# Optimization experiments

Measured on AMD Instinct MI355X. Metric: run time of the kernel, lower is better.

## Reference

```python
import math
import jax, jax.numpy as jnp
import numpy as np

B, S, D, H, FF, E, V, RH = 8, 256, 512, 8, 2048, 8, 32000, 256
MAX_PATH, MAX_VISITS = 4, 2
NEG = -1e9
DH = D // H


def _make_pe():
    # PositionalEncoding buffer (sin/cos), sliced to seq len S
    pos = np.arange(S, dtype=np.float32)[:, None]
    div = np.exp(np.arange(0, D, 2, dtype=np.float32) * (-math.log(10000.0) / D))
    pe = np.zeros((S, D), dtype=np.float32)
    pe[:, 0::2] = np.sin(pos * div)
    pe[:, 1::2] = np.cos(pos * div)
    return jnp.asarray(pe[None])  # [1,S,D]


def setup_inputs() -> dict:
    key = jax.random.key(0)
    ks = jax.random.split(key, 12)
    s = 0.02
    return dict(
        input_ids=jax.random.randint(ks[0], (B, S), 0, V),
        emb=jax.random.normal(ks[1], (V, D), jnp.float32) * s,
        pe=_make_pe(),
        Wqkv=jax.random.normal(ks[2], (E, 3 * D, D), jnp.float32) * s,
        bqkv=jnp.zeros((E, 3 * D), jnp.float32),
        Wo=jax.random.normal(ks[3], (E, D, D), jnp.float32) * s,
        bo=jnp.zeros((E, D), jnp.float32),
        W1=jax.random.normal(ks[4], (E, FF, D), jnp.float32) * s,
        b1=jnp.zeros((E, FF), jnp.float32),
        W2=jax.random.normal(ks[5], (E, D, FF), jnp.float32) * s,
        b2=jnp.zeros((E, D), jnp.float32),
        ln1_g=jnp.ones((E, D), jnp.float32), ln1_b=jnp.zeros((E, D), jnp.float32),
        ln2_g=jnp.ones((E, D), jnp.float32), ln2_b=jnp.zeros((E, D), jnp.float32),
        tag=jax.random.normal(ks[6], (E, D), jnp.float32) * 0.01,
        r_w1=jax.random.normal(ks[7], (RH, D), jnp.float32) * s,
        r_b1=jnp.zeros((RH,), jnp.float32),
        r_w2=jax.random.normal(ks[8], (E + 1, RH), jnp.float32) * s,
        r_b2=jnp.zeros((E + 1,), jnp.float32),
        lm_w=jax.random.normal(ks[9], (V, D), jnp.float32) * s,
        lm_b=jnp.zeros((V,), jnp.float32),
    )


def _ln(x, g, b):
    # per-sample gathered LayerNorm params g,b: [B,D]; x: [B,S,D]
    mu = x.mean(-1, keepdims=True)
    var = ((x - mu) ** 2).mean(-1, keepdims=True)
    return (x - mu) * jax.lax.rsqrt(var + 1e-5) * g[:, None, :] + b[:, None, :]


def _expert(x, idx, Wqkv, bqkv, Wo, bo, W1, b1, W2, b2, g1, be1, g2, be2, tag):
    # post-norm TransformerEncoderLayer (eval mode, dropout off) with per-sample expert params
    qkv = jnp.einsum('bsd,bfd->bsf', x, Wqkv[idx]) + bqkv[idx][:, None, :]
    q, k, v = jnp.split(qkv, 3, axis=-1)
    q = q.reshape(B, S, H, DH)
    k = k.reshape(B, S, H, DH)
    v = v.reshape(B, S, H, DH)
    att = jax.nn.softmax(jnp.einsum('bqhd,bkhd->bhqk', q, k) / math.sqrt(DH), axis=-1)
    ctx = jnp.einsum('bhqk,bkhd->bqhd', att, v).reshape(B, S, D)
    attn_out = jnp.einsum('bsd,bod->bso', ctx, Wo[idx]) + bo[idx][:, None, :]
    x = _ln(x + attn_out, g1[idx], be1[idx])
    hid = jax.nn.relu(jnp.einsum('bsd,bfd->bsf', x, W1[idx]) + b1[idx][:, None, :])
    ff = jnp.einsum('bsf,bdf->bsd', hid, W2[idx]) + b2[idx][:, None, :]
    x = _ln(x + ff, g2[idx], be2[idx])
    return x + tag[idx][:, None, :]  # + specialization_tag


def reference(input_ids, emb, pe, Wqkv, bqkv, Wo, bo, W1, b1, W2, b2,
              ln1_g, ln1_b, ln2_g, ln2_b, tag, r_w1, r_b1, r_w2, r_b2, lm_w, lm_b):
    pad_mask = (jnp.arange(V) != 0).astype(emb.dtype)[:, None]  # padding_idx=0 row is zero
    rep = (emb * pad_mask)[input_ids] * math.sqrt(D) + pe[:, :S]
    visits = jnp.zeros((B, E), jnp.int32)
    active = jnp.ones((B,), bool)
    ent_total = jnp.asarray(0.0, rep.dtype)
    for _ in range(MAX_PATH):
        summary = rep.mean(1)  # [B,D]
        h = jax.nn.relu(summary @ r_w1.T + r_b1)
        logits = h @ r_w2.T + r_b2  # [B,E+1], last slot = terminate
        logits = jnp.concatenate(
            [jnp.where(visits >= MAX_VISITS, NEG, logits[:, :E]), logits[:, E:]], axis=1)
        probs = jax.nn.softmax(logits, axis=-1)
        ent = -jnp.sum(probs * jnp.log(probs + 1e-9), axis=-1)
        cnt = jnp.sum(active)
        ent_total = ent_total + jnp.where(
            cnt > 0, jnp.sum(ent * active) / jnp.maximum(cnt, 1).astype(ent.dtype), 0.0)
        choice = jnp.argmax(logits, axis=-1)       # eval mode: hard argmax
        go = active & (choice < E)                 # samples routed to an expert this step
        idx = jnp.where(go, choice, 0)
        visits = visits + jax.nn.one_hot(idx, E, dtype=jnp.int32) * go[:, None].astype(jnp.int32)
        new_rep = _expert(rep, idx, Wqkv, bqkv, Wo, bo, W1, b1, W2, b2,
                          ln1_g, ln1_b, ln2_g, ln2_b, tag)
        rep = jnp.where(go[:, None, None], new_rep, rep)  # terminated/inactive reps frozen
        active = go
    logits_lm = rep @ lm_w.T + lm_b  # [B,S,V]
    return logits_lm, ent_total
```

## Files before the change

### kernel.cpp

```cpp
#include <hip/hip_runtime.h>
#include <hip/hip_bf16.h>

#define NB 8
#define NS 256
#define ND 512
#define NH 8
#define NDH 64
#define NFF 2048
#define NE 8
#define NV 32000
#define NRH 256
#define MAXV 2
#define NEGV (-1e9f)

typedef __attribute__((ext_vector_type(8))) short short8;
typedef __attribute__((ext_vector_type(4))) float f32x4;

__device__ __forceinline__ unsigned short f2bf(float x) {
  unsigned int u = __float_as_uint(x);
  u = (u + 0x7fffu + ((u >> 16) & 1u)) >> 16;
  return (unsigned short)u;
}

__device__ __forceinline__ void gload16(const unsigned short* g, unsigned short* l) {
  __builtin_amdgcn_global_load_lds(
      (const __attribute__((address_space(1))) unsigned int*)g,
      (__attribute__((address_space(3))) unsigned int*)l, 16, 0, 0);
}

__device__ __forceinline__ int swzc(int lane) {
  return (lane & 3) ^ ((lane >> 3) & 3);
}

__device__ __forceinline__ void cast8(const float* s, unsigned short* d, int j) {
  const float4* s4 = (const float4*)s;
  float4 a = s4[j * 2], b = s4[j * 2 + 1];
  short8 v;
  v[0] = (short)f2bf(a.x); v[1] = (short)f2bf(a.y);
  v[2] = (short)f2bf(a.z); v[3] = (short)f2bf(a.w);
  v[4] = (short)f2bf(b.x); v[5] = (short)f2bf(b.y);
  v[6] = (short)f2bf(b.z); v[7] = (short)f2bf(b.w);
  *(short8*)&d[(size_t)j * 8] = v;
}

__global__ __launch_bounds__(256) void k_cast5e(
    const float* s0, unsigned short* d0, int n0,
    const float* s1, unsigned short* d1, int n1,
    const float* s2, unsigned short* d2, int n2,
    const float* s3, unsigned short* d3, int n3,
    const float* s4, unsigned short* d4, int n4,
    int nbcast,
    const int* __restrict__ ids, const float* __restrict__ emb,
    const float* __restrict__ pe, float* __restrict__ rep,
    unsigned short* __restrict__ repb, float* __restrict__ partial,
    int* visits, int* active, float* entp) {
  if (blockIdx.x == 0) {
    if (threadIdx.x < NB * NE) visits[threadIdx.x] = 0;
    if (threadIdx.x < NB) active[threadIdx.x] = 1;
    if (threadIdx.x == 0) *entp = 0.f;
  }
  if ((int)blockIdx.x >= nbcast) {
    int j2 = blockIdx.x - nbcast;
    int rg = j2 & 15, b = j2 >> 4;
    int t = threadIdx.x;
    int c0 = t, c1 = t + 256;
    float pa0 = 0.f, pa1 = 0.f, pb0 = 0.f, pb1 = 0.f;
    for (int row = 0; row < 16; ++row) {
      int s = rg * 16 + row;
      int id = ids[b * NS + s];
      float sc = (id != 0) ? 22.627416997969522f : 0.f;
      float v0 = emb[(size_t)id * ND + c0] * sc + pe[(size_t)s * ND + c0];
      float v1 = emb[(size_t)id * ND + c1] * sc + pe[(size_t)s * ND + c1];
      size_t base = ((size_t)b * NS + s) * ND;
      rep[base + c0] = v0; rep[base + c1] = v1;
      repb[base + c0] = f2bf(v0); repb[base + c1] = f2bf(v1);
      if (row < 8) { pa0 += v0; pa1 += v1; } else { pb0 += v0; pb1 += v1; }
    }
    float* ppa = partial + ((size_t)b * 32 + rg * 2) * ND;
    float* ppb = ppa + ND;
    ppa[c0] = pa0; ppa[c1] = pa1;
    ppb[c0] = pb0; ppb[c1] = pb1;
    return;
  }
  int j = blockIdx.x * 256 + threadIdx.x;
  if (j < n0) { cast8(s0, d0, j); return; }
  j -= n0;
  if (j < n1) { cast8(s1, d1, j); return; }
  j -= n1;
  if (j < n2) { cast8(s2, d2, j); return; }
  j -= n2;
  if (j < n3) { cast8(s3, d3, j); return; }
  j -= n3;
  if (j < n4) cast8(s4, d4, j);
}

__global__ __launch_bounds__(256) void k_router8(
    const float* __restrict__ partial,
    const float* __restrict__ rw1, const float* __restrict__ rb1,
    const float* __restrict__ rw2, const float* __restrict__ rb2,
    int* visits, const int* __restrict__ active_in, int* active_out,
    int* idx, int* go, float* ent_total) {
  int b = blockIdx.x;
  __shared__ float sm[ND];
  __shared__ float h[NRH];
  __shared__ float lg[NE + 1];
  __shared__ int scnt;
  int t = threadIdx.x;
  for (int i = t; i < ND; i += 256) {
    const float* pp = partial + ((size_t)b * 32) * ND + i;
    float s = 0.f;
#pragma unroll
    for (int rg = 0; rg < 32; ++rg) s += pp[(size_t)rg * ND];
    sm[i] = s * (1.f / NS);
  }
  if (t == 0) {
    int c = 0;
    for (int bb = 0; bb < NB; ++bb) c += active_in[bb];
    scnt = c;
  }
  __syncthreads();
  {
    const float* w = rw1 + (size_t)t * ND;
    float acc = rb1[t];
    for (int d = 0; d < ND; ++d) acc += sm[d] * w[d];
    h[t] = fmaxf(acc, 0.f);
  }
  __syncthreads();
  if (t < NE + 1) {
    const float* w = rw2 + t * NRH;
    float a = rb2[t];
    for (int r = 0; r < NRH; ++r) a += h[r] * w[r];
    lg[t] = a;
  }
  __syncthreads();
  if (t == 0) {
    int aprev = active_in[b];
    float l[NE + 1];
    for (int e = 0; e < NE; ++e)
      l[e] = (visits[b * NE + e] >= MAXV) ? NEGV : lg[e];
    l[NE] = lg[NE];
    float m = l[0];
    for (int e = 1; e <= NE; ++e) m = fmaxf(m, l[e]);
    float z = 0.f, p[NE + 1];
    for (int e = 0; e <= NE; ++e) { p[e] = __expf(l[e] - m); z += p[e]; }
    float zi = 1.f / z, ent = 0.f;
    for (int e = 0; e <= NE; ++e) {
      float pp = p[e] * zi;
      ent -= pp * __logf(pp + 1e-9f);
    }
    if (aprev && scnt > 0) atomicAdd(ent_total, ent / (float)scnt);
    int ch = 0; float bm = l[0];
    for (int e = 1; e <= NE; ++e) if (l[e] > bm) { bm = l[e]; ch = e; }
    int g = (aprev && ch < NE) ? 1 : 0;
    int ix = g ? ch : 0;
    visits[b * NE + ix] += g;
    idx[b] = ix; go[b] = g; active_out[b] = g;
  }
}

template <int OUT, int RELU, int SK>
__global__ __launch_bounds__(256) void k_gemm64p(
    const unsigned short* __restrict__ Aall, int sa,
    const unsigned short* __restrict__ Wall, const float* __restrict__ ball,
    float* __restrict__ Pall, unsigned short* __restrict__ Uall, int so,
    int N, int K,
    unsigned short* __restrict__ Qb, unsigned short* __restrict__ Kb,
    unsigned short* __restrict__ Vt,
    const int* __restrict__ go, const int* __restrict__ idx) {
  int b = blockIdx.z;
  if (!go[b]) return;
  int t = threadIdx.x;
  int lane = t & 63, w = t >> 6;
  int wm = (w >> 1) * 32, wn = (w & 1) * 32;
  int kc = blockIdx.x >> 2;
  int bm = (blockIdx.x & 3) * 64, bn = blockIdx.y * 64;
  int KC = K / SK;
  int lrow = (lane >> 4) * 4, lcol = lane & 15;
  const unsigned short* A = Aall + (size_t)b * sa + kc * KC;
  const unsigned short* W = Wall + (size_t)idx[b] * N * K + kc * KC;

  __shared__ __align__(16) unsigned short As[2][64][64];
  __shared__ __align__(16) unsigned short Bs[2][64][64];
  f32x4 acc[2][2];
#pragma unroll
  for (int i = 0; i < 2; ++i)
#pragma unroll
    for (int j = 0; j < 2; ++j) acc[i][j] = (f32x4){0.f, 0.f, 0.f, 0.f};

  int ch8 = (lane & 7) ^ ((lane >> 3) & 7);
  const unsigned short* ga = A + (size_t)(bm + w * 16 + (lane >> 3)) * K + ch8 * 8;
  const unsigned short* gb = W + (size_t)(bn + w * 16 + (lane >> 3)) * K + ch8 * 8;

#define ISSUE64(slot, kt)                                            \
  gload16(ga + (size_t)(kt) * 64, &As[slot][w * 16][0]);             \
  gload16(ga + (size_t)(kt) * 64 + 8 * (size_t)K, &As[slot][w * 16 + 8][0]); \
  gload16(gb + (size_t)(kt) * 64, &Bs[slot][w * 16][0]);             \
  gload16(gb + (size_t)(kt) * 64 + 8 * (size_t)K, &Bs[slot][w * 16 + 8][0]);

  int nk = KC >> 6;
  ISSUE64(0, 0)
  ISSUE64(1, 1)

  int row0 = lane & 15, g = lane >> 4;
  for (int it = 0; it < nk; ++it) {
    if (it < nk - 1) asm volatile("s_waitcnt vmcnt(4)" ::: "memory");
    else             asm volatile("s_waitcnt vmcnt(0)" ::: "memory");
    asm volatile("s_barrier" ::: "memory");
    int sl = it & 1;
    __builtin_amdgcn_s_setprio(1);
#pragma unroll
    for (int kk = 0; kk < 2; ++kk) {
      int co = ((kk * 4 + g) ^ (row0 & 7)) * 8;
      short8 a0 = *(const short8*)&As[sl][wm + row0][co];
      short8 a1 = *(const short8*)&As[sl][wm + 16 + row0][co];
      short8 b0 = *(const short8*)&Bs[sl][wn + row0][co];
      short8 b1 = *(const short8*)&Bs[sl][wn + 16 + row0][co];
      acc[0][0] = __builtin_amdgcn_mfma_f32_16x16x32_bf16(a0, b0, acc[0][0], 0, 0, 0);
      acc[0][1] = __builtin_amdgcn_mfma_f32_16x16x32_bf16(a0, b1, acc[0][1], 0, 0, 0);
      acc[1][0] = __builtin_amdgcn_mfma_f32_16x16x32_bf16(a1, b0, acc[1][0], 0, 0, 0);
      acc[1][1] = __builtin_amdgcn_mfma_f32_16x16x32_bf16(a1, b1, acc[1][1], 0, 0, 0);
    }
    __builtin_amdgcn_s_setprio(0);
    asm volatile("s_barrier" ::: "memory");
    if (it + 2 < nk) { ISSUE64(sl, it + 2) }
  }
#undef ISSUE64

  if (OUT == 2) {
    const float* bias = ball + (size_t)idx[b] * N;
    int seg = bn >> 9;
#pragma unroll
    for (int nf = 0; nf < 2; ++nf) {
      int col = bn + wn + nf * 16 + lcol;
      float bv = bias[col];
      if (seg < 2) {
        unsigned short* dst = (seg == 0) ? Qb : Kb;
        int cc = col - seg * 512;
#pragma unroll
        for (int mf = 0; mf < 2; ++mf)
#pragma unroll
          for (int r = 0; r < 4; ++r) {
            int row = bm + wm + mf * 16 + lrow + r;
            dst[((size_t)b * NS + row) * ND + cc] = f2bf(acc[mf][nf][r] + bv);
          }
      } else {
        int dcol = col - 1024;
#pragma unroll
        for (int mf = 0; mf < 2; ++mf) {
          int s0 = bm + wm + mf * 16 + lrow;
          unsigned long long pk =
              (unsigned long long)f2bf(acc[mf][nf][0] + bv) |
              ((unsigned long long)f2bf(acc[mf][nf][1] + bv) << 16) |
              ((unsigned long long)f2bf(acc[mf][nf][2] + bv) << 32) |
              ((unsigned long long)f2bf(acc[mf][nf][3] + bv) << 48);
          *(unsigned long long*)&Vt[((size_t)b * 512 + dcol) * 256 + s0] = pk;
        }
      }
    }
  } else if (OUT == 1) {
    const float* bias = ball + (size_t)idx[b] * N;
#pragma unroll
    for (int nf = 0; nf < 2; ++nf) {
      int col = bn + wn + nf * 16 + lcol;
      float bv = bias[col];
#pragma unroll
      for (int mf = 0; mf < 2; ++mf) {
#pragma unroll
        for (int r = 0; r < 4; ++r) {
          int row = bm + wm + mf * 16 + lrow + r;
          float v = acc[mf][nf][r] + bv;
          if (RELU) v = fmaxf(v, 0.f);
          Uall[(size_t)b * so + (size_t)row * N + col] = f2bf(v);
        }
      }
    }
  } else {
    float* P = Pall + ((size_t)kc * NB + b) * ((size_t)NS * N);
#pragma unroll
    for (int nf = 0; nf < 2; ++nf) {
      int col = bn + wn + nf * 16 + lcol;
#pragma unroll
      for (int mf = 0; mf < 2; ++mf)
#pragma unroll
        for (int r = 0; r < 4; ++r)
          P[(size_t)(bm + wm + mf * 16 + lrow + r) * N + col] = acc[mf][nf][r];
    }
  }
}

__global__ __launch_bounds__(256) void k_attn2(const unsigned short* __restrict__ Qb,
                                               const unsigned short* __restrict__ Kb,
                                               const unsigned short* __restrict__ Vt,
                                               unsigned short* __restrict__ ctxb,
                                               const int* __restrict__ go) {
  int b = blockIdx.z, h = blockIdx.y, qt = blockIdx.x;
  if (!go[b]) return;
  int t = threadIdx.x;
  __shared__ __align__(16) unsigned short lds0[16384];
  __shared__ __align__(16) unsigned short lds1[16384];
  int lane = t & 63, w = t >> 6, g = lane >> 4, c = lane & 15;

#pragma unroll
  for (int i = 0; i < 8; ++i) {
    int task = i * 256 + t;
    int k = task >> 3, cc = task & 7;
    short8 v = *(const short8*)&Kb[((size_t)b * NS + k) * ND + h * NDH + cc * 8];
    *(short8*)&lds0[k * 64 + ((cc * 8) ^ ((k & 7) << 3))] = v;
  }
#pragma unroll
  for (int i = 0; i < 8; ++i) {
    int task = i * 256 + t;
    int d = task >> 5, kc = task & 31;
    short8 v = *(const short8*)&Vt[((size_t)b * 512 + h * NDH + d) * 256 + kc * 8];
    *(short8*)&lds1[d * 256 + ((kc * 8) ^ ((d & 7) << 3))] = v;
  }
  short8 qf[2];
  {
    const unsigned short* qp = Qb + ((size_t)b * NS + qt * 64 + w * 16 + c) * ND + h * NDH;
    qf[0] = *(const short8*)&qp[g * 8];
    qf[1] = *(const short8*)&qp[32 + g * 8];
  }
  __syncthreads();

  f32x4 sacc[16];
#pragma unroll
  for (int mf = 0; mf < 16; ++mf) sacc[mf] = (f32x4){0.f, 0.f, 0.f, 0.f};
#pragma unroll
  for (int mf = 0; mf < 16; ++mf) {
#pragma unroll
    for (int kd = 0; kd < 2; ++kd) {
      int row = mf * 16 + c;
      short8 kf = *(const short8*)&lds0[row * 64 + ((kd * 32 + g * 8) ^ ((row & 7) << 3))];
      sacc[mf] = __builtin_amdgcn_mfma_f32_16x16x32_bf16(kf, qf[kd], sacc[mf], 0, 0, 0);
    }
  }
  __syncthreads();

  float mx = -3.4e38f;
#pragma unroll
  for (int mf = 0; mf < 16; ++mf) {
#pragma unroll
    for (int r = 0; r < 4; ++r) {
      sacc[mf][r] *= 0.125f;
      mx = fmaxf(mx, sacc[mf][r]);
    }
  }
  mx = fmaxf(mx, __shfl_xor(mx, 16));
  mx = fmaxf(mx, __shfl_xor(mx, 32));
  float sum = 0.f;
#pragma unroll
  for (int mf = 0; mf < 16; ++mf)
#pragma unroll
    for (int r = 0; r < 4; ++r) {
      float p = __expf(sacc[mf][r] - mx);
      sacc[mf][r] = p;
      sum += p;
    }
  sum += __shfl_xor(sum, 16);
  sum += __shfl_xor(sum, 32);
  float zi = 1.f / sum;

  int q_l = w * 16 + c;
#pragma unroll
  for (int mf = 0; mf < 16; ++mf) {
    unsigned long long pk =
        (unsigned long long)f2bf(sacc[mf][0] * zi) |
        ((unsigned long long)f2bf(sacc[mf][1] * zi) << 16) |
        ((unsigned long long)f2bf(sacc[mf][2] * zi) << 32) |
        ((unsigned long long)f2bf(sacc[mf][3] * zi) << 48);
    *(unsigned long long*)&lds0[q_l * 256 + ((mf * 16 + g * 4) ^ ((q_l & 7) << 3))] = pk;
  }

  f32x4 cacc[4];
#pragma unroll
  for (int nf = 0; nf < 4; ++nf) cacc[nf] = (f32x4){0.f, 0.f, 0.f, 0.f};
#pragma unroll
  for (int ks = 0; ks < 8; ++ks) {
    int prow = w * 16 + c;
    short8 pf = *(const short8*)&lds0[prow * 256 + ((ks * 32 + g * 8) ^ ((prow & 7) << 3))];
#pragma unroll
    for (int nf = 0; nf < 4; ++nf) {
      int vrow = nf * 16 + c;
      short8 vf = *(const short8*)&lds1[vrow * 256 + ((ks * 32 + g * 8) ^ ((vrow & 7) << 3))];
      cacc[nf] = __builtin_amdgcn_mfma_f32_16x16x32_bf16(pf, vf, cacc[nf], 0, 0, 0);
    }
  }
#pragma unroll
  for (int nf = 0; nf < 4; ++nf)
#pragma unroll
    for (int r = 0; r < 4; ++r)
      ctxb[((size_t)b * NS + qt * 64 + w * 16 + g * 4 + r) * ND + h * NDH + nf * 16 + c] =
          f2bf(cacc[nf][r]);
}

template <int NCH, int TAG, int SUMP>
__global__ __launch_bounds__(256) void k_ln_red(
    const float* __restrict__ res, const float* __restrict__ part,
    const float* __restrict__ gbias,
    const float* __restrict__ gall, const float* __restrict__ beall,
    const float* __restrict__ tagall,
    float* __restrict__ outf, unsigned short* __restrict__ outb,
    float* __restrict__ sump,
    const int* __restrict__ go, const int* __restrict__ idx) {
  int b = blockIdx.y;
  if (!go[b]) return;
  int rg = blockIdx.x;
  int w = threadIdx.x >> 6, l = threadIdx.x & 63;
  int ix = idx[b];
  int d = l * 8;
  float gb8[8], gg[8], bb[8];
  {
    float4 a0 = *(const float4*)&gbias[ix * ND + d];
    float4 a1 = *(const float4*)&gbias[ix * ND + d + 4];
    gb8[0] = a0.x; gb8[1] = a0.y; gb8[2] = a0.z; gb8[3] = a0.w;
    gb8[4] = a1.x; gb8[5] = a1.y; gb8[6] = a1.z; gb8[7] = a1.w;
    float4 g0 = *(const float4*)&gall[ix * ND + d];
    float4 g1 = *(const float4*)&gall[ix * ND + d + 4];
    gg[0] = g0.x; gg[1] = g0.y; gg[2] = g0.z; gg[3] = g0.w;
    gg[4] = g1.x; gg[5] = g1.y; gg[6] = g1.z; gg[7] = g1.w;
    float4 b0 = *(const float4*)&beall[ix * ND + d];
    float4 b1 = *(const float4*)&beall[ix * ND + d + 4];
    bb[0] = b0.x; bb[1] = b0.y; bb[2] = b0.z; bb[3] = b0.w;
    bb[4] = b1.x; bb[5] = b1.y; bb[6] = b1.z; bb[7] = b1.w;
    if (TAG) {
      float4 t0 = *(const float4*)&tagall[ix * ND + d];
      float4 t1 = *(const float4*)&tagall[ix * ND + d + 4];
      bb[0] += t0.x; bb[1] += t0.y; bb[2] += t0.z; bb[3] += t0.w;
      bb[4] += t1.x; bb[5] += t1.y; bb[6] += t1.z; bb[7] += t1.w;
    }
  }
  float ps[8] = {0.f, 0.f, 0.f, 0.f, 0.f, 0.f, 0.f, 0.f};
  const size_t CSTRIDE = (size_t)NB * NS * ND;
  for (int rr = 0; rr < 2; ++rr) {
    int s = rg * 8 + w * 2 + rr;
    size_t base = ((size_t)b * NS + s) * ND;
    float4 x0 = *(const float4*)&res[base + d];
    float4 x1 = *(const float4*)&res[base + d + 4];
    float v[8] = {x0.x + gb8[0], x0.y + gb8[1], x0.z + gb8[2], x0.w + gb8[3],
                  x1.x + gb8[4], x1.y + gb8[5], x1.z + gb8[6], x1.w + gb8[7]};
#pragma unroll
    for (int c = 0; c < NCH; ++c) {
      const float* pc = part + c * CSTRIDE + base;
      float4 p0 = *(const float4*)&pc[d];
      float4 p1 = *(const float4*)&pc[d + 4];
      v[0] += p0.x; v[1] += p0.y; v[2] += p0.z; v[3] += p0.w;
      v[4] += p1.x; v[5] += p1.y; v[6] += p1.z; v[7] += p1.w;
    }
    float sum = 0.f;
#pragma unroll
    for (int j = 0; j < 8; ++j) sum += v[j];
#pragma unroll
    for (int off = 1; off < 64; off <<= 1) sum += __shfl_xor(sum, off);
    float mu = sum * (1.f / ND);
    float var = 0.f;
#pragma unroll
    for (int j = 0; j < 8; ++j) { v[j] -= mu; var += v[j] * v[j]; }
#pragma unroll
    for (int off = 1; off < 64; off <<= 1) var += __shfl_xor(var, off);
    float rs = rsqrtf(var * (1.f / ND) + 1e-5f);
    float o[8];
    short8 ob;
#pragma unroll
    for (int j = 0; j < 8; ++j) {
      o[j] = v[j] * rs * gg[j] + bb[j];
      if (SUMP) ps[j] += o[j];
      ob[j] = (short)f2bf(o[j]);
    }
    *(float4*)&outf[base + d] = (float4){o[0], o[1], o[2], o[3]};
    *(float4*)&outf[base + d + 4] = (float4){o[4], o[5], o[6], o[7]};
    *(short8*)&outb[base + d] = ob;
  }
  if (SUMP) {
    __shared__ float pl[4][ND];
#pragma unroll
    for (int j = 0; j < 8; ++j) pl[w][d + j] = ps[j];
    __syncthreads();
    if (w == 0) {
      float* pp = sump + ((size_t)b * 32 + rg) * ND;
#pragma unroll
      for (int j = 0; j < 8; ++j)
        pp[d + j] = pl[0][d + j] + pl[1][d + j] + pl[2][d + j] + pl[3][d + j];
    }
  }
}

__global__ __launch_bounds__(512, 2) void k_lmhead256(const unsigned short* __restrict__ Ab,
                                                      const unsigned short* __restrict__ Wb,
                                                      const float* __restrict__ bias,
                                                      float* __restrict__ out,
                                                      const float* __restrict__ entp) {
  if (blockIdx.x == 0 && threadIdx.x == 0)
    out[(size_t)NB * NS * NV] = *entp;
  int id = blockIdx.x;
  int swz = (id & 7) * 125 + (id >> 3);
  int bm = (swz % 8) * 256;
  int bn = (swz / 8) * 256;

  __shared__ __align__(16) unsigned short As[2][256][32];
  __shared__ __align__(16) unsigned short Bs[2][256][32];
  int t = threadIdx.x;
  int lane = t & 63, w = t >> 6;
  int wm = (w >> 2) * 128, wn = (w & 3) * 64;
  f32x4 acc[8][4];
#pragma unroll
  for (int i = 0; i < 8; ++i)
#pragma unroll
    for (int j = 0; j < 4; ++j) acc[i][j] = (f32x4){0.f, 0.f, 0.f, 0.f};

  const unsigned short* ga = Ab + (size_t)(bm + w * 32 + (lane >> 2)) * ND + swzc(lane) * 8;
  const unsigned short* gb = Wb + (size_t)(bn + w * 32 + (lane >> 2)) * ND + swzc(lane) * 8;

#define ISSUEL(slot, kt)                                           \
  gload16(ga + (kt) * 32, &As[slot][w * 32][0]);                   \
  gload16(ga + (kt) * 32 + 16 * ND, &As[slot][w * 32 + 16][0]);    \
  gload16(gb + (kt) * 32, &Bs[slot][w * 32][0]);                   \
  gload16(gb + (kt) * 32 + 16 * ND, &Bs[slot][w * 32 + 16][0]);

  ISSUEL(0, 0)
  ISSUEL(1, 1)

  int row0 = lane & 15;
  int cs = ((lane >> 4) ^ ((row0 >> 1) & 3)) * 8;
  for (int it = 0; it < 16; ++it) {
    if (it < 15) asm volatile("s_waitcnt vmcnt(4)" ::: "memory");
    else         asm volatile("s_waitcnt vmcnt(0)" ::: "memory");
    asm volatile("s_barrier" ::: "memory");
    int sl = it & 1;
    short8 a[8], bfr[4];
#pragma unroll
    for (int mf = 0; mf < 8; ++mf)
      a[mf] = *(const short8*)&As[sl][wm + mf * 16 + row0][cs];
#pragma unroll
    for (int nf = 0; nf < 4; ++nf)
      bfr[nf] = *(const short8*)&Bs[sl][wn + nf * 16 + row0][cs];
    __builtin_amdgcn_s_setprio(1);
#pragma unroll
    for (int mf = 0; mf < 8; ++mf)
#pragma unroll
      for (int nf = 0; nf < 4; ++nf)
        acc[mf][nf] = __builtin_amdgcn_mfma_f32_16x16x32_bf16(a[mf], bfr[nf], acc[mf][nf], 0, 0, 0);
    __builtin_amdgcn_s_setprio(0);
    asm volatile("s_barrier" ::: "memory");
    if (it + 2 < 16) { ISSUEL(sl, it + 2) }
  }
#undef ISSUEL

  int lrow = (lane >> 4) * 4, lcol = lane & 15;
#pragma unroll
  for (int nf = 0; nf < 4; ++nf) {
    int col = bn + wn + nf * 16 + lcol;
    float bv = bias[col];
#pragma unroll
    for (int mf = 0; mf < 8; ++mf) {
#pragma unroll
      for (int r = 0; r < 4; ++r) {
        int row = bm + wm + mf * 16 + lrow + r;
        out[(size_t)row * NV + col] = acc[mf][nf][r] + bv;
      }
    }
  }
}

extern "C" void kernel_launch(void* const* d_in, const int* in_sizes, int n_in,
                              void* d_out, int out_size, void* d_ws, size_t ws_size,
                              hipStream_t stream) {
  const int* ids   = (const int*)d_in[0];
  const float* emb = (const float*)d_in[1];
  const float* pe  = (const float*)d_in[2];
  const float* Wqkv = (const float*)d_in[3];
  const float* bqkv = (const float*)d_in[4];
  const float* Wo   = (const float*)d_in[5];
  const float* bo   = (const float*)d_in[6];
  const float* W1   = (const float*)d_in[7];
  const float* b1   = (const float*)d_in[8];
  const float* W2   = (const float*)d_in[9];
  const float* b2   = (const float*)d_in[10];
  const float* g1   = (const float*)d_in[11];
  const float* be1  = (const float*)d_in[12];
  const float* g2   = (const float*)d_in[13];
  const float* be2  = (const float*)d_in[14];
  const float* tag  = (const float*)d_in[15];
  const float* rw1  = (const float*)d_in[16];
  const float* rb1  = (const float*)d_in[17];
  const float* rw2  = (const float*)d_in[18];
  const float* rb2  = (const float*)d_in[19];
  const float* lmw  = (const float*)d_in[20];
  const float* lmb  = (const float*)d_in[21];
  float* out = (float*)d_out;

  float* ws = (float*)d_ws;
  size_t o = 0;
  float* rep = ws + o;  o += (size_t)NB * NS * ND;
  float* x1  = ws + o;  o += (size_t)NB * NS * ND;
  float* partk = ws + o; o += (size_t)4 * NB * NS * ND;
  float* partial = ws + o; o += (size_t)NB * 32 * ND;
  int* visits = (int*)(ws + o); o += 1024;
  int* active0 = visits + NB * NE;
  int* active1 = active0 + NB;
  int* idx = active1 + NB;
  int* go = idx + NB;
  float* entp = (float*)(go + NB);

  unsigned short* us = (unsigned short*)(ws + o);
  size_t uo = 0;
  unsigned short* rep_b = us + uo; uo += (size_t)NB * NS * ND;
  unsigned short* x1_b  = us + uo; uo += (size_t)NB * NS * ND;
  unsigned short* ctx_b = us + uo; uo += (size_t)NB * NS * ND;
  unsigned short* Qb    = us + uo; uo += (size_t)NB * NS * ND;
  unsigned short* Kb    = us + uo; uo += (size_t)NB * NS * ND;
  unsigned short* Vt    = us + uo; uo += (size_t)NB * NS * ND;
  unsigned short* hid_b = us + uo; uo += (size_t)NB * NS * NFF;
  unsigned short* Wqkv_b = us + uo; uo += (size_t)NE * 3 * ND * ND;
  unsigned short* Wo_b   = us + uo; uo += (size_t)NE * ND * ND;
  unsigned short* W1_b   = us + uo; uo += (size_t)NE * NFF * ND;
  unsigned short* W2_b   = us + uo; uo += (size_t)NE * ND * NFF;
  unsigned short* lmw_b  = us + uo; uo += (size_t)NV * ND;

  {
    int n0 = NE * 3 * ND * ND / 8, n1 = NE * ND * ND / 8, n2 = NE * NFF * ND / 8,
        n3 = NE * ND * NFF / 8, n4 = NV * ND / 8;
    int nbcast = (n0 + n1 + n2 + n3 + n4) / 256;
    k_cast5e<<<nbcast + 16 * NB, 256, 0, stream>>>(
        Wqkv, Wqkv_b, n0, Wo, Wo_b, n1, W1, W1_b, n2, W2, W2_b, n3, lmw, lmw_b, n4,
        nbcast, ids, emb, pe, rep, rep_b, partial, visits, active0, entp);
  }

  for (int step = 0; step < 4; ++step) {
    int* act_in  = (step & 1) ? active1 : active0;
    int* act_out = (step & 1) ? active0 : active1;
    k_router8<<<NB, 256, 0, stream>>>(partial, rw1, rb1, rw2, rb2,
                                      visits, act_in, act_out, idx, go, entp);
    k_gemm64p<2, 0, 1><<<dim3(4, 24, NB), 256, 0, stream>>>(
        rep_b, NS * ND, Wqkv_b, bqkv, nullptr, nullptr, 0, 3 * ND, ND,
        Qb, Kb, Vt, go, idx);
    k_attn2<<<dim3(4, NH, NB), 256, 0, stream>>>(Qb, Kb, Vt, ctx_b, go);
    k_gemm64p<0, 0, 2><<<dim3(8, 8, NB), 256, 0, stream>>>(
        ctx_b, NS * ND, Wo_b, nullptr, partk, nullptr, 0, ND, ND,
        nullptr, nullptr, nullptr, go, idx);
    k_ln_red<2, 0, 0><<<dim3(32, NB), 256, 0, stream>>>(
        rep, partk, bo, g1, be1, nullptr, x1, x1_b, nullptr, go, idx);
    k_gemm64p<1, 1, 1><<<dim3(4, 32, NB), 256, 0, stream>>>(
        x1_b, NS * ND, W1_b, b1, nullptr, hid_b, NS * NFF, NFF, ND,
        nullptr, nullptr, nullptr, go, idx);
    k_gemm64p<0, 0, 4><<<dim3(16, 8, NB), 256, 0, stream>>>(
        hid_b, NS * NFF, W2_b, nullptr, partk, nullptr, 0, ND, NFF,
        nullptr, nullptr, nullptr, go, idx);
    k_ln_red<4, 1, 1><<<dim3(32, NB), 256, 0, stream>>>(
        x1, partk, b2, g2, be2, tag, rep, rep_b, partial, go, idx);
  }

  k_lmhead256<<<1000, 512, 0, stream>>>(rep_b, lmw_b, lmb, out, entp);
}
```

Before: 507.0 us.

## Drop fp32 residual copies, keep residual stream in bf16; read V directly from global in attention

Removes the fp32 rep and x1 buffers, so the LayerNorm kernels read the residual from its bf16 copy and write only bf16. This cuts fp32 global traffic and stores in the embedding, LN1 and LN2 stages. Separately, the attention kernel no longer stages V into shared memory: it reads V fragments straight from global, adds a barrier before the PV step, and uses half as much LDS. The residual now carries bf16 rounding through every layer, which changes numerical accuracy, and the uncached global V reads may cost more latency than the LDS staging did.

```diff
diff --git a/kernel.cpp b/kernel.cpp
--- a/kernel.cpp
+++ b/kernel.cpp
@@ -21,6 +21,9 @@
   u = (u + 0x7fffu + ((u >> 16) & 1u)) >> 16;
   return (unsigned short)u;
 }
+__device__ __forceinline__ float bf2f(unsigned short x) {
+  return __uint_as_float(((unsigned int)x) << 16);
+}
 
 __device__ __forceinline__ void gload16(const unsigned short* g, unsigned short* l) {
   __builtin_amdgcn_global_load_lds(
@@ -51,7 +54,7 @@
     const float* s4, unsigned short* d4, int n4,
     int nbcast,
     const int* __restrict__ ids, const float* __restrict__ emb,
-    const float* __restrict__ pe, float* __restrict__ rep,
+    const float* __restrict__ pe,
     unsigned short* __restrict__ repb, float* __restrict__ partial,
     int* visits, int* active, float* entp) {
   if (blockIdx.x == 0) {
@@ -72,7 +75,6 @@
       float v0 = emb[(size_t)id * ND + c0] * sc + pe[(size_t)s * ND + c0];
       float v1 = emb[(size_t)id * ND + c1] * sc + pe[(size_t)s * ND + c1];
       size_t base = ((size_t)b * NS + s) * ND;
-      rep[base + c0] = v0; rep[base + c1] = v1;
       repb[base + c0] = f2bf(v0); repb[base + c1] = f2bf(v1);
       if (row < 8) { pa0 += v0; pa1 += v1; } else { pb0 += v0; pb1 += v1; }
     }
@@ -297,7 +299,6 @@
   if (!go[b]) return;
   int t = threadIdx.x;
   __shared__ __align__(16) unsigned short lds0[16384];
-  __shared__ __align__(16) unsigned short lds1[16384];
   int lane = t & 63, w = t >> 6, g = lane >> 4, c = lane & 15;
 
 #pragma unroll
@@ -306,13 +307,6 @@
     int k = task >> 3, cc = task & 7;
     short8 v = *(const short8*)&Kb[((size_t)b * NS + k) * ND + h * NDH + cc * 8];
     *(short8*)&lds0[k * 64 + ((cc * 8) ^ ((k & 7) << 3))] = v;
-  }
-#pragma unroll
-  for (int i = 0; i < 8; ++i) {
-    int task = i * 256 + t;
-    int d = task >> 5, kc = task & 31;
-    short8 v = *(const short8*)&Vt[((size_t)b * 512 + h * NDH + d) * 256 + kc * 8];
-    *(short8*)&lds1[d * 256 + ((kc * 8) ^ ((d & 7) << 3))] = v;
   }
   short8 qf[2];
   {
@@ -370,18 +364,19 @@
         ((unsigned long long)f2bf(sacc[mf][3] * zi) << 48);
     *(unsigned long long*)&lds0[q_l * 256 + ((mf * 16 + g * 4) ^ ((q_l & 7) << 3))] = pk;
   }
+  __syncthreads();
 
   f32x4 cacc[4];
 #pragma unroll
   for (int nf = 0; nf < 4; ++nf) cacc[nf] = (f32x4){0.f, 0.f, 0.f, 0.f};
+  const unsigned short* vbase = Vt + ((size_t)b * 512 + h * NDH) * 256;
 #pragma unroll
   for (int ks = 0; ks < 8; ++ks) {
     int prow = w * 16 + c;
     short8 pf = *(const short8*)&lds0[prow * 256 + ((ks * 32 + g * 8) ^ ((prow & 7) << 3))];
 #pragma unroll
     for (int nf = 0; nf < 4; ++nf) {
-      int vrow = nf * 16 + c;
-      short8 vf = *(const short8*)&lds1[vrow * 256 + ((ks * 32 + g * 8) ^ ((vrow & 7) << 3))];
+      short8 vf = *(const short8*)&vbase[(size_t)(nf * 16 + c) * 256 + ks * 32 + g * 8];
       cacc[nf] = __builtin_amdgcn_mfma_f32_16x16x32_bf16(pf, vf, cacc[nf], 0, 0, 0);
     }
   }
@@ -395,11 +390,11 @@
 
 template <int NCH, int TAG, int SUMP>
 __global__ __launch_bounds__(256) void k_ln_red(
-    const float* __restrict__ res, const float* __restrict__ part,
+    const unsigned short* __restrict__ resb, const float* __restrict__ part,
     const float* __restrict__ gbias,
     const float* __restrict__ gall, const float* __restrict__ beall,
     const float* __restrict__ tagall,
-    float* __restrict__ outf, unsigned short* __restrict__ outb,
+    unsigned short* __restrict__ outb,
     float* __restrict__ sump,
     const int* __restrict__ go, const int* __restrict__ idx) {
   int b = blockIdx.y;
@@ -434,10 +429,10 @@
   for (int rr = 0; rr < 2; ++rr) {
     int s = rg * 8 + w * 2 + rr;
     size_t base = ((size_t)b * NS + s) * ND;
-    float4 x0 = *(const float4*)&res[base + d];
-    float4 x1 = *(const float4*)&res[base + d + 4];
-    float v[8] = {x0.x + gb8[0], x0.y + gb8[1], x0.z + gb8[2], x0.w + gb8[3],
-                  x1.x + gb8[4], x1.y + gb8[5], x1.z + gb8[6], x1.w + gb8[7]};
+    short8 xr = *(const short8*)&resb[base + d];
+    float v[8];
+#pragma unroll
+    for (int j = 0; j < 8; ++j) v[j] = bf2f((unsigned short)xr[j]) + gb8[j];
 #pragma unroll
     for (int c = 0; c < NCH; ++c) {
       const float* pc = part + c * CSTRIDE + base;
@@ -466,8 +461,6 @@
       if (SUMP) ps[j] += o[j];
       ob[j] = (short)f2bf(o[j]);
     }
-    *(float4*)&outf[base + d] = (float4){o[0], o[1], o[2], o[3]};
-    *(float4*)&outf[base + d + 4] = (float4){o[4], o[5], o[6], o[7]};
     *(short8*)&outb[base + d] = ob;
   }
   if (SUMP) {
@@ -590,8 +583,6 @@
 
   float* ws = (float*)d_ws;
   size_t o = 0;
-  float* rep = ws + o;  o += (size_t)NB * NS * ND;
-  float* x1  = ws + o;  o += (size_t)NB * NS * ND;
   float* partk = ws + o; o += (size_t)4 * NB * NS * ND;
   float* partial = ws + o; o += (size_t)NB * 32 * ND;
   int* visits = (int*)(ws + o); o += 1024;
@@ -622,7 +613,7 @@
     int nbcast = (n0 + n1 + n2 + n3 + n4) / 256;
     k_cast5e<<<nbcast + 16 * NB, 256, 0, stream>>>(
         Wqkv, Wqkv_b, n0, Wo, Wo_b, n1, W1, W1_b, n2, W2, W2_b, n3, lmw, lmw_b, n4,
-        nbcast, ids, emb, pe, rep, rep_b, partial, visits, active0, entp);
+        nbcast, ids, emb, pe, rep_b, partial, visits, active0, entp);
   }
 
   for (int step = 0; step < 4; ++step) {
@@ -638,7 +629,7 @@
         ctx_b, NS * ND, Wo_b, nullptr, partk, nullptr, 0, ND, ND,
         nullptr, nullptr, nullptr, go, idx);
     k_ln_red<2, 0, 0><<<dim3(32, NB), 256, 0, stream>>>(
-        rep, partk, bo, g1, be1, nullptr, x1, x1_b, nullptr, go, idx);
+        rep_b, partk, bo, g1, be1, nullptr, x1_b, nullptr, go, idx);
     k_gemm64p<1, 1, 1><<<dim3(4, 32, NB), 256, 0, stream>>>(
         x1_b, NS * ND, W1_b, b1, nullptr, hid_b, NS * NFF, NFF, ND,
         nullptr, nullptr, nullptr, go, idx);
@@ -646,7 +637,7 @@
         hid_b, NS * NFF, W2_b, nullptr, partk, nullptr, 0, ND, NFF,
         nullptr, nullptr, nullptr, go, idx);
     k_ln_red<4, 1, 1><<<dim3(32, NB), 256, 0, stream>>>(
-        x1, partk, b2, g2, be2, tag, rep, rep_b, partial, go, idx);
+        x1_b, partk, b2, g2, be2, tag, rep_b, partial, go, idx);
   }
 
   k_lmhead256<<<1000, 512, 0, stream>>>(rep_b, lmw_b, lmb, out, entp);
```

Result: no change. 505.2 us (-0.4%).
